# Optimization experiments

Measured on AMD Instinct MI355X. Metric: run time of the kernel, lower is better.

## Reference

```python
import jax, jax.numpy as jnp
import numpy as np
import math

# Spherical conv per Esteves et al. spherical CNNs (sph_conv_batch):
#   1) spherical-harmonic transform of input on an n x n equiangular grid
#   2) per-degree multiply by zonal filter coeffs w[c_in, l, c_out],
#      scaled by 2*pi*sqrt(4*pi/(2l+1))
#   3) inverse transform, plus bias add.
# Implemented as FFT over longitude + Legendre quadrature over colatitude.

BATCH, N_GRID, C_IN, C_OUT = 64, 32, 128, 128
L_MAX = N_GRID // 2  # spherical-harmonic bandwidth


def _legendre_Q(L, n):
    """Normalized associated Legendre N_lm * P_l^m(cos theta_j).
    Returns Q (L, 2L-1, n) with m index offset by L-1, and theta (n,)."""
    theta = np.pi * (np.arange(n) + 0.5) / n
    x, sx = np.cos(theta), np.sin(theta)
    P = np.zeros((L, L, n))
    P[0, 0] = 1.0
    for m in range(1, L):
        P[m, m] = -(2 * m - 1) * sx * P[m - 1, m - 1]
    for m in range(L - 1):
        P[m + 1, m] = (2 * m + 1) * x * P[m, m]
        for l in range(m + 2, L):
            P[l, m] = ((2 * l - 1) * x * P[l - 1, m] - (l + m - 1) * P[l - 2, m]) / (l - m)
    Q = np.zeros((L, 2 * L - 1, n))
    for l in range(L):
        for m in range(l + 1):
            Nlm = np.sqrt((2 * l + 1) / (4 * np.pi)
                          * np.exp(math.lgamma(l - m + 1) - math.lgamma(l + m + 1)))
            Q[l, L - 1 + m] = Nlm * P[l, m]
            Q[l, L - 1 - m] = ((-1) ** m) * Nlm * P[l, m]
    return Q, theta


def _sph_conv(inputs, weights, bias):
    b, n, _, c_in = inputs.shape
    L = weights.shape[1]
    Q, theta = _legendre_Q(L, n)
    # quadrature: sin(theta)*dtheta*dphi, dtheta = pi/n, dphi = 2*pi/n
    wj = np.sin(theta) * (np.pi / n) * (2.0 * np.pi / n)
    Qw = jnp.asarray(Q * wj, dtype=jnp.float32).astype(jnp.complex64)   # (L, 2L-1, n)
    Qs = jnp.asarray(Q, dtype=jnp.float32).astype(jnp.complex64)
    ms = np.arange(-(L - 1), L) % n  # 2L-1 distinct FFT bins
    # forward SHT: FFT over phi then Legendre quadrature over theta
    F = jnp.fft.fft(inputs.astype(jnp.complex64), axis=2)[:, :, ms, :]  # (b, n, 2L-1, c_in)
    coef = jnp.einsum('lmj,bjmc->blmc', Qw, F)                          # (b, L, 2L-1, c_in)
    # zonal spectral filter: per-degree scale 2*pi*sqrt(4*pi/(2l+1))
    scale = jnp.asarray(2.0 * np.pi * np.sqrt(4.0 * np.pi / (2.0 * np.arange(L) + 1.0)),
                        jnp.float32)
    chat = jnp.einsum('blmi,ilo->blmo', coef, weights.astype(jnp.complex64))
    chat = chat * scale[None, :, None, None]
    # inverse SHT: Legendre synthesis then inverse FFT over phi
    G = jnp.einsum('blmo,lmj->bjmo', chat, Qs)                          # (b, n, 2L-1, c_out)
    Gfull = jnp.zeros((b, n, n, G.shape[-1]), jnp.complex64).at[:, :, ms, :].set(G)
    out = jnp.real(jnp.fft.ifft(Gfull, axis=2)) * n                    # (b, n, n, c_out)
    return out + bias


def setup_inputs() -> dict:
    key = jax.random.key(0)
    k1, k2 = jax.random.split(key)
    std = 2.0 / (2.0 * np.pi * np.sqrt(L_MAX * C_IN))
    inputs = jax.random.normal(k1, (BATCH, N_GRID, N_GRID, C_IN), jnp.float32)
    weights = jax.random.normal(k2, (C_IN, L_MAX, C_OUT), jnp.float32) * std
    bias = jnp.zeros((1, 1, 1, C_OUT), jnp.float32)
    return {"inputs": inputs, "weights": weights, "bias": bias}


def reference(inputs, weights, bias):
    return _sph_conv(inputs, weights, bias)
```

## Files before the change

### kernel.cpp

```cpp
#include <hip/hip_runtime.h>
#include <hip/hip_bf16.h>
#include <math.h>


#define NPAIR 136
#define PADC 140

typedef __attribute__((ext_vector_type(8))) short short8;
typedef __attribute__((ext_vector_type(4))) float f32x4;
#define MFMA16(A, B, C) __builtin_amdgcn_mfma_f32_16x16x32_bf16(A, B, C, 0, 0, 0)

static __device__ __forceinline__ float us2f(unsigned int u) {
  union { unsigned int i; float f; } v; v.i = u << 16; return v.f;
}
static __device__ __forceinline__ unsigned short f2us(float f) {
  __hip_bfloat16 h = __float2bfloat16(f);
  return *(unsigned short*)&h;
}
static __device__ __forceinline__ float lo_f(unsigned int pk) {
  union { unsigned int i; float f; } v; v.i = pk << 16; return v.f;
}
static __device__ __forceinline__ float hi_f(unsigned int pk) {
  union { unsigned int i; float f; } v; v.i = pk & 0xffff0000u; return v.f;
}
static __device__ __forceinline__ unsigned int packbf(float a, float b) {
  return (unsigned int)f2us(a) | ((unsigned int)f2us(b) << 16);
}

__device__ __align__(16) unsigned short g_atab_h[NPAIR * 32];
__device__ __align__(16) float          g_stab[32 * PADC];
__device__ int g_tab_ready;

static __device__ __forceinline__ int detect_fp32(const void* xin) {
  const unsigned short* u = (const unsigned short*)xin;
  int lane = threadIdx.x & 63;
  int big = 0;
#pragma unroll
  for (int q = 0; q < 4; ++q) {
    float v = us2f((unsigned int)u[lane * 8 + q * 2]);
    if (!(fabsf(v) <= 1e3f)) big = 1;
  }
  unsigned long long mask = __ballot(big);
  return (__popcll(mask) >= 16) ? 1 : 0;
}

static __device__ __forceinline__ size_t chat_q_byte(int b, int oq, int u, int esz) {
  int wpr = 8 * esz;
  int s = u / wpr, w = u % wpr;
  return ((size_t)b * 131072 + (size_t)s * 128 + oq * 32) * (size_t)esz + (size_t)w * 4;
}
static __device__ __forceinline__ size_t coef_byte(int b, int h, int u, int esz) {
  int wpr = 16 * esz;
  int s = 544 / esz + u / wpr, w = u % wpr;
  return ((size_t)b * 131072 + (size_t)s * 128 + h * 64) * (size_t)esz + (size_t)w * 4;
}

#define DEF_TRIG \
  constexpr float CT[32] = { \
    1.0f, 0.98078528f, 0.92387953f, 0.83146961f, 0.70710678f, 0.55557023f, \
    0.38268343f, 0.19509032f, 0.0f, -0.19509032f, -0.38268343f, -0.55557023f, \
    -0.70710678f, -0.83146961f, -0.92387953f, -0.98078528f, -1.0f, \
    -0.98078528f, -0.92387953f, -0.83146961f, -0.70710678f, -0.55557023f, \
    -0.38268343f, -0.19509032f, 0.0f, 0.19509032f, 0.38268343f, 0.55557023f, \
    0.70710678f, 0.83146961f, 0.92387953f, 0.98078528f }; \
  constexpr float ST[32] = { \
    0.0f, 0.19509032f, 0.38268343f, 0.55557023f, 0.70710678f, 0.83146961f, \
    0.92387953f, 0.98078528f, 1.0f, 0.98078528f, 0.92387953f, 0.83146961f, \
    0.70710678f, 0.55557023f, 0.38268343f, 0.19509032f, 0.0f, \
    -0.19509032f, -0.38268343f, -0.55557023f, -0.70710678f, -0.83146961f, \
    -0.92387953f, -0.98078528f, -1.0f, -0.98078528f, -0.92387953f, \
    -0.83146961f, -0.70710678f, -0.55557023f, -0.38268343f, -0.19509032f }

__global__ void k_init() {
  if (g_tab_ready) return;
  const int pair = blockIdx.x, j = threadIdx.x;
  int m = 0;
#pragma unroll
  for (int mm = 1; mm < 16; ++mm) {
    int off = mm * 16 - (mm * (mm - 1)) / 2;
    if (off <= pair) m = mm;
  }
  const int l = m + (pair - (m * 16 - (m * (m - 1)) / 2));
  double theta = M_PI * (j + 0.5) / 32.0;
  double x = cos(theta), sx = sin(theta);
  double wj = sx * (M_PI / 32.0) * (2.0 * M_PI / 32.0);
  double pmm = 1.0;
  for (int k = 1; k <= m; ++k) pmm *= -(2.0 * k - 1.0) * sx;
  double p = pmm, pl1 = 0.0, pl2 = 0.0;
  for (int ll = m; ll <= l; ++ll) {
    if (ll == m)          p = pmm;
    else if (ll == m + 1) p = (2.0 * m + 1.0) * x * pmm;
    else                  p = ((2.0 * ll - 1.0) * x * pl1 - (double)(ll + m - 1) * pl2) / (double)(ll - m);
    pl2 = pl1; pl1 = p;
  }
  double r = 1.0;
  for (int k = l - m + 1; k <= l + m; ++k) r *= (double)k;
  double Nlm = sqrt((2.0 * l + 1.0) / (4.0 * M_PI) / r);
  g_atab_h[pair * 32 + j] = f2us((float)(Nlm * p * wj));
  g_stab[j * PADC + pair] = (float)(Nlm * p * (2.0 * M_PI * sqrt(4.0 * M_PI / (2.0 * l + 1.0)))
                                    * (m ? 2.0 : 1.0));
  if (pair == NPAIR - 1 && j == 31) g_tab_ready = 1;
}

__global__ __launch_bounds__(256) void k_fwd(const void* __restrict__ xin,
                                             char* __restrict__ outbuf) {
  const int fp32m = detect_fp32(xin);
  const int esz = fp32m ? 4 : 2;
  __shared__ __align__(16) unsigned short xs[32 * 264];
  __shared__ __align__(16) unsigned int   fsp[128 * 36];
  const int blk = blockIdx.x;
  const int b = (blk & 7) | (((blk >> 7) & 7) << 3);
  const int cq = (blk >> 3) & 15;
  const int t = threadIdx.x;
  uint4 at0 = ((const uint4*)g_atab_h)[t];
  uint4 at1 = ((const uint4*)g_atab_h)[t + 256];
  uint4 at2;
  if (t < 32) at2 = ((const uint4*)g_atab_h)[512 + t];
  if (fp32m) {
    const float* xf = (const float*)xin;
#pragma unroll
    for (int it = 0; it < 8; ++it) {
      int i = t + it * 256;
      int s = i >> 1, hf = i & 1;
      float4 v = *(const float4*)(xf + ((size_t)b * 1024 + s) * 128 + cq * 8 + hf * 4);
      int p = s & 31, j = s >> 5;
      *(uint2*)&xs[p * 264 + j * 8 + hf * 4] = make_uint2(packbf(v.x, v.y), packbf(v.z, v.w));
    }
  } else {
    const unsigned short* xh = (const unsigned short*)xin;
#pragma unroll
    for (int it = 0; it < 4; ++it) {
      int s = t + it * 256;
      uint4 v = *(const uint4*)(xh + ((size_t)b * 1024 + s) * 128 + cq * 8);
      int p = s & 31, j = s >> 5;
      *(uint4*)&xs[p * 264 + j * 8] = v;
    }
  }
  __syncthreads();
  {
    DEF_TRIG;
    const int j = t >> 3, c = t & 7, rb = j * 8 + c;
    float x0  = us2f((unsigned int)xs[rb]);
    float x16 = us2f((unsigned int)xs[16 * 264 + rb]);
    float sp[16], dm[16];
#pragma unroll
    for (int p = 1; p <= 15; ++p) {
      float a  = us2f((unsigned int)xs[p * 264 + rb]);
      float bq = us2f((unsigned int)xs[(32 - p) * 264 + rb]);
      sp[p] = a + bq; dm[p] = a - bq;
    }
#pragma unroll
    for (int mi = 0; mi < 16; ++mi) {
      float re = x0 + ((mi & 1) ? -x16 : x16);
      float im = 0.f;
#pragma unroll
      for (int p = 1; p <= 15; ++p) {
        re += sp[p] * CT[(mi * p) & 31];
        im -= dm[p] * ST[(mi * p) & 31];
      }
      fsp[(mi * 8 + c) * 36 + j] = packbf(re, im);
    }
  }
  __syncthreads();
  ((uint4*)xs)[t] = at0;
  ((uint4*)xs)[t + 256] = at1;
  if (t < 32) ((uint4*)xs)[512 + t] = at2;
  __syncthreads();
  {
    const int m = t >> 4, c = (t >> 1) & 7, jh = t & 1;
    const int cg = cq * 8 + c, h = cg >> 6, cl = cg & 63;
    const int base = m * 16 - (m * (m - 1)) / 2;
    uint4 F[4];
#pragma unroll
    for (int q = 0; q < 4; ++q)
      F[q] = *(const uint4*)&fsp[(m * 8 + c) * 36 + jh * 16 + q * 4];
    for (int l = m; l < 16; ++l) {
      int pair = base + (l - m);
      float sr = 0.f, si = 0.f;
#pragma unroll
      for (int q = 0; q < 2; ++q) {
        uint4 a = ((const uint4*)xs)[pair * 4 + jh * 2 + q];
        float a0 = us2f(a.x & 0xffff), a1 = us2f(a.x >> 16);
        float a2 = us2f(a.y & 0xffff), a3 = us2f(a.y >> 16);
        float a4 = us2f(a.z & 0xffff), a5 = us2f(a.z >> 16);
        float a6 = us2f(a.w & 0xffff), a7 = us2f(a.w >> 16);
        uint4 f0 = F[2 * q], f1 = F[2 * q + 1];
        sr += a0 * lo_f(f0.x) + a1 * lo_f(f0.y) + a2 * lo_f(f0.z) + a3 * lo_f(f0.w)
            + a4 * lo_f(f1.x) + a5 * lo_f(f1.y) + a6 * lo_f(f1.z) + a7 * lo_f(f1.w);
        si += a0 * hi_f(f0.x) + a1 * hi_f(f0.y) + a2 * hi_f(f0.z) + a3 * hi_f(f0.w)
            + a4 * hi_f(f1.x) + a5 * hi_f(f1.y) + a6 * hi_f(f1.z) + a7 * hi_f(f1.w);
      }
      sr += __shfl_xor(sr, 1, 64);
      si += __shfl_xor(si, 1, 64);
      if (jh == 0) {
        int u = pair * 64 + cl;
        *(unsigned int*)(outbuf + coef_byte(b, h, u, esz)) = packbf(sr, si);
      }
    }
  }
}

__global__ __launch_bounds__(256) void k_chan(char* __restrict__ outbuf,
                                              const void* __restrict__ Wv,
                                              const void* __restrict__ xin) {
  const int fp32m = detect_fp32(xin);
  const int esz = fp32m ? 4 : 2;
  const int pair = blockIdx.x >> 2;
  const int bh = (blockIdx.x >> 1) & 1, otile = blockIdx.x & 1;
  int m = 0;
#pragma unroll
  for (int mm = 1; mm < 16; ++mm) {
    int off = mm * 16 - (mm * (mm - 1)) / 2;
    if (off <= pair) m = mm;
  }
  const int l = m + (pair - (m * 16 - (m * (m - 1)) / 2));
  __shared__ __align__(16) unsigned short Xr[32 * 136];
  __shared__ __align__(16) unsigned short Xi[32 * 136];
  __shared__ __align__(16) unsigned short Wt[64 * 136];
  const int t = threadIdx.x;
  for (int i = t; i < 1024; i += 256) {
    int bl = i >> 5, c4 = (i & 31) * 4;
    uint4 pk = *(const uint4*)(outbuf +
        coef_byte(bh * 32 + bl, c4 >> 6, pair * 64 + (c4 & 63), esz));
    Xr[bl * 136 + c4 + 0] = (unsigned short)(pk.x & 0xffff);
    Xi[bl * 136 + c4 + 0] = (unsigned short)(pk.x >> 16);
    Xr[bl * 136 + c4 + 1] = (unsigned short)(pk.y & 0xffff);
    Xi[bl * 136 + c4 + 1] = (unsigned short)(pk.y >> 16);
    Xr[bl * 136 + c4 + 2] = (unsigned short)(pk.z & 0xffff);
    Xi[bl * 136 + c4 + 2] = (unsigned short)(pk.z >> 16);
    Xr[bl * 136 + c4 + 3] = (unsigned short)(pk.w & 0xffff);
    Xi[bl * 136 + c4 + 3] = (unsigned short)(pk.w >> 16);
  }
  for (int i = t; i < 1024; i += 256) {
    int c = i >> 3, og = i & 7;
    size_t widx = (size_t)c * 2048 + l * 128 + otile * 64 + og * 8;
    if (fp32m) {
      const float* Wf = (const float*)Wv;
      float4 f0 = *(const float4*)(Wf + widx);
      float4 f1 = *(const float4*)(Wf + widx + 4);
      Wt[(og * 8 + 0) * 136 + c] = f2us(f0.x); Wt[(og * 8 + 1) * 136 + c] = f2us(f0.y);
      Wt[(og * 8 + 2) * 136 + c] = f2us(f0.z); Wt[(og * 8 + 3) * 136 + c] = f2us(f0.w);
      Wt[(og * 8 + 4) * 136 + c] = f2us(f1.x); Wt[(og * 8 + 5) * 136 + c] = f2us(f1.y);
      Wt[(og * 8 + 6) * 136 + c] = f2us(f1.z); Wt[(og * 8 + 7) * 136 + c] = f2us(f1.w);
    } else {
      const unsigned short* Wh = (const unsigned short*)Wv;
      uint4 v = *(const uint4*)(Wh + widx);
      Wt[(og * 8 + 0) * 136 + c] = (unsigned short)(v.x & 0xffff);
      Wt[(og * 8 + 1) * 136 + c] = (unsigned short)(v.x >> 16);
      Wt[(og * 8 + 2) * 136 + c] = (unsigned short)(v.y & 0xffff);
      Wt[(og * 8 + 3) * 136 + c] = (unsigned short)(v.y >> 16);
      Wt[(og * 8 + 4) * 136 + c] = (unsigned short)(v.z & 0xffff);
      Wt[(og * 8 + 5) * 136 + c] = (unsigned short)(v.z >> 16);
      Wt[(og * 8 + 6) * 136 + c] = (unsigned short)(v.w & 0xffff);
      Wt[(og * 8 + 7) * 136 + c] = (unsigned short)(v.w >> 16);
    }
  }
  __syncthreads();
  const int wv = t >> 6, lane = t & 63;
  const int col = lane & 15, quad = lane >> 4;
  const int mtile = wv & 1, ng = wv >> 1;
  f32x4 accR0 = {0.f, 0.f, 0.f, 0.f}, accI0 = accR0, accR1 = accR0, accI1 = accR0;
#pragma unroll
  for (int kc = 0; kc < 4; ++kc) {
    short8 Ar = *(const short8*)&Xr[(mtile * 16 + col) * 136 + kc * 32 + quad * 8];
    short8 Ai = *(const short8*)&Xi[(mtile * 16 + col) * 136 + kc * 32 + quad * 8];
    short8 B0 = *(const short8*)&Wt[(ng * 32 + col) * 136 + kc * 32 + quad * 8];
    short8 B1 = *(const short8*)&Wt[(ng * 32 + 16 + col) * 136 + kc * 32 + quad * 8];
    accR0 = MFMA16(Ar, B0, accR0);
    accI0 = MFMA16(Ai, B0, accI0);
    accR1 = MFMA16(Ar, B1, accR1);
    accI1 = MFMA16(Ai, B1, accI1);
  }
#pragma unroll
  for (int reg = 0; reg < 4; ++reg) {
    int bb = bh * 32 + mtile * 16 + quad * 4 + reg;
    int o0 = otile * 64 + ng * 32 + col;
    int o1 = o0 + 16;
    *(unsigned int*)(outbuf + chat_q_byte(bb, o0 >> 5, pair * 32 + (o0 & 31), esz)) =
        packbf(accR0[reg], accI0[reg]);
    *(unsigned int*)(outbuf + chat_q_byte(bb, o1 >> 5, pair * 32 + (o1 & 31), esz)) =
        packbf(accR1[reg], accI1[reg]);
  }
}

__global__ __launch_bounds__(1024) void k_bwd(char* __restrict__ outbuf,
                                              const void* __restrict__ biasv,
                                              const void* __restrict__ xin) {
  const int fp32m = detect_fp32(xin);
  const int esz = fp32m ? 4 : 2;
  __shared__ __align__(16) unsigned int chs[32 * PADC];
  __shared__ __align__(16) float        stb[32 * PADC];
  const int b = blockIdx.x >> 2, oq = blockIdx.x & 3;
  const int t = threadIdx.x;
  for (int i = t; i < NPAIR * 8; i += 1024) {
    uint4 v = *(const uint4*)(outbuf + chat_q_byte(b, oq, i * 4, esz));
    const int pair = i >> 3, ol0 = (i & 7) * 4;
    chs[(ol0 + 0) * PADC + pair] = v.x;
    chs[(ol0 + 1) * PADC + pair] = v.y;
    chs[(ol0 + 2) * PADC + pair] = v.z;
    chs[(ol0 + 3) * PADC + pair] = v.w;
  }
  for (int i = t; i < 32 * PADC / 4; i += 1024)
    ((float4*)stb)[i] = ((const float4*)g_stab)[i];
  const int j = t >> 5, ol = t & 31;
  const int o = oq * 32 + ol;
  const float bv = fp32m ? ((const float*)biasv)[o]
                         : us2f((unsigned int)((const unsigned short*)biasv)[o]);
  __syncthreads();

  float Gr[16], Gi[16];
#pragma unroll
  for (int mm = 0; mm < 16; ++mm) { Gr[mm] = 0.f; Gi[mm] = 0.f; }
  {
    float4 s4 = {0.f, 0.f, 0.f, 0.f};
    uint4  c4 = {0u, 0u, 0u, 0u};
    int pair = 0;
#pragma unroll
    for (int mm = 0; mm < 16; ++mm) {
#pragma unroll
      for (int l = mm; l < 16; ++l) {
        if ((pair & 3) == 0) {
          s4 = *(const float4*)&stb[j * PADC + pair];
          c4 = *(const uint4*)&chs[ol * PADC + pair];
        }
        const int r = pair & 3;
        const float        s  = (r == 0) ? s4.x : (r == 1) ? s4.y : (r == 2) ? s4.z : s4.w;
        const unsigned int cv = (r == 0) ? c4.x : (r == 1) ? c4.y : (r == 2) ? c4.z : c4.w;
        Gr[mm] += s * lo_f(cv);
        Gi[mm] += s * hi_f(cv);
        ++pair;
      }
    }
  }
  DEF_TRIG;
#pragma unroll
  for (int pp = 0; pp <= 16; ++pp) {
    float A = 0.f, Bv = 0.f;
#pragma unroll
    for (int mm = 0; mm < 16; ++mm) {
      A  += Gr[mm] * CT[(mm * pp) & 31];
      Bv += Gi[mm] * ST[(mm * pp) & 31];
    }
    const int p2 = (32 - pp) & 31;
    size_t e1 = (size_t)b * 131072 + (size_t)(j * 32 + pp) * 128 + o;
    size_t e2 = (size_t)b * 131072 + (size_t)(j * 32 + p2) * 128 + o;
    if (fp32m) {
      *(float*)(outbuf + e1 * 4) = bv + A - Bv;
      *(float*)(outbuf + e2 * 4) = bv + A + Bv;
    } else {
      *(unsigned short*)(outbuf + e1 * 2) = f2us(bv + A - Bv);
      *(unsigned short*)(outbuf + e2 * 2) = f2us(bv + A + Bv);
    }
  }
}

extern "C" void kernel_launch(void* const* d_in, const int* in_sizes, int n_in,
                              void* d_out, int out_size, void* d_ws, size_t ws_size,
                              hipStream_t stream) {
  const void* xin  = d_in[0];
  const void* W    = d_in[1];
  const void* bias = d_in[2];
  char* out = (char*)d_out;

  hipLaunchKernelGGL(k_init, dim3(NPAIR), dim3(32),   0, stream);
  hipLaunchKernelGGL(k_fwd,  dim3(1024),  dim3(256),  0, stream, xin, out);
  hipLaunchKernelGGL(k_chan, dim3(544),   dim3(256),  0, stream, out, W, xin);
  hipLaunchKernelGGL(k_bwd,  dim3(256),   dim3(1024), 0, stream, out, bias, xin);
}
```

Measured before the change: 118.1 us.

## Fuse channel-mixing MFMA into backward synthesis kernel and use workspace for coefficients

The channel-mixing GEMM kernel is folded into the backward Legendre/iFFT kernel. Each of the 16 waves handles one degree l, loads the weights for its l and output quarter into registers, and writes the mixed coefficients straight into shared memory. Forward coefficients now go to a simple linear workspace instead of a packed region of the output buffer. This removes one launch and a global round-trip of intermediate spectra. In exchange, every block reloads weights with strided scalar loads, and each block recomputes the mixing for its batch item only.

```diff
diff --git a/kernel.cpp b/kernel.cpp
--- a/kernel.cpp
+++ b/kernel.cpp
@@ -42,17 +42,6 @@
   }
   unsigned long long mask = __ballot(big);
   return (__popcll(mask) >= 16) ? 1 : 0;
-}
-
-static __device__ __forceinline__ size_t chat_q_byte(int b, int oq, int u, int esz) {
-  int wpr = 8 * esz;
-  int s = u / wpr, w = u % wpr;
-  return ((size_t)b * 131072 + (size_t)s * 128 + oq * 32) * (size_t)esz + (size_t)w * 4;
-}
-static __device__ __forceinline__ size_t coef_byte(int b, int h, int u, int esz) {
-  int wpr = 16 * esz;
-  int s = 544 / esz + u / wpr, w = u % wpr;
-  return ((size_t)b * 131072 + (size_t)s * 128 + h * 64) * (size_t)esz + (size_t)w * 4;
 }
 
 #define DEF_TRIG \
@@ -103,9 +92,8 @@
 }
 
 __global__ __launch_bounds__(256) void k_fwd(const void* __restrict__ xin,
-                                             char* __restrict__ outbuf) {
+                                             unsigned int* __restrict__ ws) {
   const int fp32m = detect_fp32(xin);
-  const int esz = fp32m ? 4 : 2;
   __shared__ __align__(16) unsigned short xs[32 * 264];
   __shared__ __align__(16) unsigned int   fsp[128 * 36];
   const int blk = blockIdx.x;
@@ -168,7 +156,7 @@
   __syncthreads();
   {
     const int m = t >> 4, c = (t >> 1) & 7, jh = t & 1;
-    const int cg = cq * 8 + c, h = cg >> 6, cl = cg & 63;
+    const int cg = cq * 8 + c;
     const int base = m * 16 - (m * (m - 1)) / 2;
     uint4 F[4];
 #pragma unroll
@@ -192,116 +180,88 @@
       }
       sr += __shfl_xor(sr, 1, 64);
       si += __shfl_xor(si, 1, 64);
-      if (jh == 0) {
-        int u = pair * 64 + cl;
-        *(unsigned int*)(outbuf + coef_byte(b, h, u, esz)) = packbf(sr, si);
-      }
-    }
-  }
-}
-
-__global__ __launch_bounds__(256) void k_chan(char* __restrict__ outbuf,
-                                              const void* __restrict__ Wv,
-                                              const void* __restrict__ xin) {
+      if (jh == 0)
+        ws[((size_t)b * NPAIR + pair) * 128 + cg] = packbf(sr, si);
+    }
+  }
+}
+
+__global__ __launch_bounds__(1024, 4) void k_cb(const unsigned int* __restrict__ ws,
+                                                char* __restrict__ outbuf,
+                                                const void* __restrict__ Wv,
+                                                const void* __restrict__ biasv,
+                                                const void* __restrict__ xin) {
   const int fp32m = detect_fp32(xin);
-  const int esz = fp32m ? 4 : 2;
-  const int pair = blockIdx.x >> 2;
-  const int bh = (blockIdx.x >> 1) & 1, otile = blockIdx.x & 1;
-  int m = 0;
-#pragma unroll
-  for (int mm = 1; mm < 16; ++mm) {
-    int off = mm * 16 - (mm * (mm - 1)) / 2;
-    if (off <= pair) m = mm;
-  }
-  const int l = m + (pair - (m * 16 - (m * (m - 1)) / 2));
-  __shared__ __align__(16) unsigned short Xr[32 * 136];
-  __shared__ __align__(16) unsigned short Xi[32 * 136];
-  __shared__ __align__(16) unsigned short Wt[64 * 136];
-  const int t = threadIdx.x;
-  for (int i = t; i < 1024; i += 256) {
-    int bl = i >> 5, c4 = (i & 31) * 4;
-    uint4 pk = *(const uint4*)(outbuf +
-        coef_byte(bh * 32 + bl, c4 >> 6, pair * 64 + (c4 & 63), esz));
-    Xr[bl * 136 + c4 + 0] = (unsigned short)(pk.x & 0xffff);
-    Xi[bl * 136 + c4 + 0] = (unsigned short)(pk.x >> 16);
-    Xr[bl * 136 + c4 + 1] = (unsigned short)(pk.y & 0xffff);
-    Xi[bl * 136 + c4 + 1] = (unsigned short)(pk.y >> 16);
-    Xr[bl * 136 + c4 + 2] = (unsigned short)(pk.z & 0xffff);
-    Xi[bl * 136 + c4 + 2] = (unsigned short)(pk.z >> 16);
-    Xr[bl * 136 + c4 + 3] = (unsigned short)(pk.w & 0xffff);
-    Xi[bl * 136 + c4 + 3] = (unsigned short)(pk.w >> 16);
-  }
-  for (int i = t; i < 1024; i += 256) {
-    int c = i >> 3, og = i & 7;
-    size_t widx = (size_t)c * 2048 + l * 128 + otile * 64 + og * 8;
-    if (fp32m) {
-      const float* Wf = (const float*)Wv;
-      float4 f0 = *(const float4*)(Wf + widx);
-      float4 f1 = *(const float4*)(Wf + widx + 4);
-      Wt[(og * 8 + 0) * 136 + c] = f2us(f0.x); Wt[(og * 8 + 1) * 136 + c] = f2us(f0.y);
-      Wt[(og * 8 + 2) * 136 + c] = f2us(f0.z); Wt[(og * 8 + 3) * 136 + c] = f2us(f0.w);
-      Wt[(og * 8 + 4) * 136 + c] = f2us(f1.x); Wt[(og * 8 + 5) * 136 + c] = f2us(f1.y);
-      Wt[(og * 8 + 6) * 136 + c] = f2us(f1.z); Wt[(og * 8 + 7) * 136 + c] = f2us(f1.w);
-    } else {
-      const unsigned short* Wh = (const unsigned short*)Wv;
-      uint4 v = *(const uint4*)(Wh + widx);
-      Wt[(og * 8 + 0) * 136 + c] = (unsigned short)(v.x & 0xffff);
-      Wt[(og * 8 + 1) * 136 + c] = (unsigned short)(v.x >> 16);
-      Wt[(og * 8 + 2) * 136 + c] = (unsigned short)(v.y & 0xffff);
-      Wt[(og * 8 + 3) * 136 + c] = (unsigned short)(v.y >> 16);
-      Wt[(og * 8 + 4) * 136 + c] = (unsigned short)(v.z & 0xffff);
-      Wt[(og * 8 + 5) * 136 + c] = (unsigned short)(v.z >> 16);
-      Wt[(og * 8 + 6) * 136 + c] = (unsigned short)(v.w & 0xffff);
-      Wt[(og * 8 + 7) * 136 + c] = (unsigned short)(v.w >> 16);
-    }
-  }
-  __syncthreads();
-  const int wv = t >> 6, lane = t & 63;
-  const int col = lane & 15, quad = lane >> 4;
-  const int mtile = wv & 1, ng = wv >> 1;
-  f32x4 accR0 = {0.f, 0.f, 0.f, 0.f}, accI0 = accR0, accR1 = accR0, accI1 = accR0;
-#pragma unroll
-  for (int kc = 0; kc < 4; ++kc) {
-    short8 Ar = *(const short8*)&Xr[(mtile * 16 + col) * 136 + kc * 32 + quad * 8];
-    short8 Ai = *(const short8*)&Xi[(mtile * 16 + col) * 136 + kc * 32 + quad * 8];
-    short8 B0 = *(const short8*)&Wt[(ng * 32 + col) * 136 + kc * 32 + quad * 8];
-    short8 B1 = *(const short8*)&Wt[(ng * 32 + 16 + col) * 136 + kc * 32 + quad * 8];
-    accR0 = MFMA16(Ar, B0, accR0);
-    accI0 = MFMA16(Ai, B0, accI0);
-    accR1 = MFMA16(Ar, B1, accR1);
-    accI1 = MFMA16(Ai, B1, accI1);
-  }
-#pragma unroll
-  for (int reg = 0; reg < 4; ++reg) {
-    int bb = bh * 32 + mtile * 16 + quad * 4 + reg;
-    int o0 = otile * 64 + ng * 32 + col;
-    int o1 = o0 + 16;
-    *(unsigned int*)(outbuf + chat_q_byte(bb, o0 >> 5, pair * 32 + (o0 & 31), esz)) =
-        packbf(accR0[reg], accI0[reg]);
-    *(unsigned int*)(outbuf + chat_q_byte(bb, o1 >> 5, pair * 32 + (o1 & 31), esz)) =
-        packbf(accR1[reg], accI1[reg]);
-  }
-}
-
-__global__ __launch_bounds__(1024) void k_bwd(char* __restrict__ outbuf,
-                                              const void* __restrict__ biasv,
-                                              const void* __restrict__ xin) {
-  const int fp32m = detect_fp32(xin);
-  const int esz = fp32m ? 4 : 2;
   __shared__ __align__(16) unsigned int chs[32 * PADC];
   __shared__ __align__(16) float        stb[32 * PADC];
   const int b = blockIdx.x >> 2, oq = blockIdx.x & 3;
   const int t = threadIdx.x;
-  for (int i = t; i < NPAIR * 8; i += 1024) {
-    uint4 v = *(const uint4*)(outbuf + chat_q_byte(b, oq, i * 4, esz));
-    const int pair = i >> 3, ol0 = (i & 7) * 4;
-    chs[(ol0 + 0) * PADC + pair] = v.x;
-    chs[(ol0 + 1) * PADC + pair] = v.y;
-    chs[(ol0 + 2) * PADC + pair] = v.z;
-    chs[(ol0 + 3) * PADC + pair] = v.w;
-  }
   for (int i = t; i < 32 * PADC / 4; i += 1024)
     ((float4*)stb)[i] = ((const float4*)g_stab)[i];
+  {
+    const int lw = t >> 6, lane = t & 63;
+    const int col = lane & 15, quad = lane >> 4;
+    const int s = col;
+    const int av = (s <= lw);
+    const int pv = av ? (s * 16 - (s * (s - 1)) / 2 + (lw - s)) : 0;
+    short8 Bf[2][4];
+    if (fp32m) {
+      const float* Wf = (const float*)Wv;
+#pragma unroll
+      for (int nt = 0; nt < 2; ++nt) {
+        const float* wp = Wf + (size_t)lw * 128 + oq * 32 + nt * 16 + col;
+#pragma unroll
+        for (int kc = 0; kc < 4; ++kc)
+#pragma unroll
+          for (int r = 0; r < 8; ++r)
+            ((unsigned short*)&Bf[nt][kc])[r] =
+                f2us(wp[(size_t)(kc * 32 + quad * 8 + r) * 2048]);
+      }
+    } else {
+      const unsigned short* Wh = (const unsigned short*)Wv;
+#pragma unroll
+      for (int nt = 0; nt < 2; ++nt) {
+        const unsigned short* wp = Wh + (size_t)lw * 128 + oq * 32 + nt * 16 + col;
+#pragma unroll
+        for (int kc = 0; kc < 4; ++kc)
+#pragma unroll
+          for (int r = 0; r < 8; ++r)
+            ((unsigned short*)&Bf[nt][kc])[r] = wp[(size_t)(kc * 32 + quad * 8 + r) * 2048];
+      }
+    }
+    f32x4 aR0 = {0.f, 0.f, 0.f, 0.f}, aI0 = aR0, aR1 = aR0, aI1 = aR0;
+#pragma unroll
+    for (int kc = 0; kc < 4; ++kc) {
+      uint4 u0 = {0u, 0u, 0u, 0u}, u1 = u0;
+      if (av) {
+        const unsigned int* cp = ws + ((size_t)b * NPAIR + pv) * 128 + kc * 32 + quad * 8;
+        u0 = *(const uint4*)cp;
+        u1 = *(const uint4*)(cp + 4);
+      }
+      short8 Ar, Ai;
+      Ar[0] = (short)(u0.x & 0xffff); Ai[0] = (short)(u0.x >> 16);
+      Ar[1] = (short)(u0.y & 0xffff); Ai[1] = (short)(u0.y >> 16);
+      Ar[2] = (short)(u0.z & 0xffff); Ai[2] = (short)(u0.z >> 16);
+      Ar[3] = (short)(u0.w & 0xffff); Ai[3] = (short)(u0.w >> 16);
+      Ar[4] = (short)(u1.x & 0xffff); Ai[4] = (short)(u1.x >> 16);
+      Ar[5] = (short)(u1.y & 0xffff); Ai[5] = (short)(u1.y >> 16);
+      Ar[6] = (short)(u1.z & 0xffff); Ai[6] = (short)(u1.z >> 16);
+      Ar[7] = (short)(u1.w & 0xffff); Ai[7] = (short)(u1.w >> 16);
+      aR0 = MFMA16(Ar, Bf[0][kc], aR0);
+      aI0 = MFMA16(Ai, Bf[0][kc], aI0);
+      aR1 = MFMA16(Ar, Bf[1][kc], aR1);
+      aI1 = MFMA16(Ai, Bf[1][kc], aI1);
+    }
+#pragma unroll
+    for (int reg = 0; reg < 4; ++reg) {
+      int slot = quad * 4 + reg;
+      if (slot <= lw) {
+        int pp_ = slot * 16 - (slot * (slot - 1)) / 2 + (lw - slot);
+        chs[(0 * 16 + col) * PADC + pp_] = packbf(aR0[reg], aI0[reg]);
+        chs[(1 * 16 + col) * PADC + pp_] = packbf(aR1[reg], aI1[reg]);
+      }
+    }
+  }
   const int j = t >> 5, ol = t & 31;
   const int o = oq * 32 + ol;
   const float bv = fp32m ? ((const float*)biasv)[o]
@@ -361,9 +321,9 @@
   const void* W    = d_in[1];
   const void* bias = d_in[2];
   char* out = (char*)d_out;
+  unsigned int* ws = (unsigned int*)d_ws;
 
   hipLaunchKernelGGL(k_init, dim3(NPAIR), dim3(32),   0, stream);
-  hipLaunchKernelGGL(k_fwd,  dim3(1024),  dim3(256),  0, stream, xin, out);
-  hipLaunchKernelGGL(k_chan, dim3(544),   dim3(256),  0, stream, out, W, xin);
-  hipLaunchKernelGGL(k_bwd,  dim3(256),   dim3(1024), 0, stream, out, bias, xin);
-}
+  hipLaunchKernelGGL(k_fwd,  dim3(1024),  dim3(256),  0, stream, xin, ws);
+  hipLaunchKernelGGL(k_cb,   dim3(256),   dim3(1024), 0, stream, ws, out, W, bias, xin);
+}
```

Result: faster. 114.3 us (-3.2%).
